# Kernel tuning notes

Measured on AMD Instinct MI355X. Metric: run time of the kernel, lower is better.

The kernel has to match this reference:

```python
import jax, jax.numpy as jnp
import numpy as np

B, N, C = 2, 2048, 1024
H = 16
D = C // H  # 64 head_dim
SCALE = D ** -0.5


def setup_inputs() -> dict:
    key = jax.random.key(0)
    k1, k2, k3 = jax.random.split(key, 3)
    x = jax.random.normal(k1, (B, N, C), dtype=jnp.float32)
    w_qkv = jax.random.normal(k2, (C, 3 * C), dtype=jnp.float32) * (C ** -0.5)
    w_proj = jax.random.normal(k3, (C, C), dtype=jnp.float32) * (C ** -0.5)
    b_proj = jnp.zeros((C,), dtype=jnp.float32)
    return {"x": x, "w_qkv": w_qkv, "w_proj": w_proj, "b_proj": b_proj}


def reference(x, w_qkv, w_proj, b_proj):
    # qkv projection (no bias, qkv_bias=False)
    qkv = x @ w_qkv                                   # [B,N,3C]
    qkv = qkv.reshape(B, N, 3, H, D)
    qkv = jnp.transpose(qkv, (2, 0, 3, 1, 4))         # [3,B,H,N,D]
    q, k, v = qkv[0], qkv[1], qkv[2]
    # scaled dot-product attention (full softmax == chunked loop in original)
    scores = jnp.einsum('bhqd,bhkd->bhqk', q, k) * SCALE
    attn = jax.nn.softmax(scores, axis=-1)
    out = jnp.einsum('bhqk,bhkd->bhqd', attn, v)      # [B,H,N,D]
    out = jnp.transpose(out, (0, 2, 1, 3)).reshape(B, N, C)
    return out @ w_proj + b_proj
```

## Files before the change

kernel.cpp:

```cpp
#include <hip/hip_runtime.h>
#include <stdint.h>

typedef float f32x4 __attribute__((ext_vector_type(4)));
typedef float f32x16 __attribute__((ext_vector_type(16)));
typedef __bf16 bf16x8 __attribute__((ext_vector_type(8)));
typedef unsigned int u32x4 __attribute__((ext_vector_type(4)));
typedef unsigned short u16x4 __attribute__((ext_vector_type(4)));

#define DEV __device__ __forceinline__

#define QSCALE_LOG2E 0.18033688011112042f

DEV unsigned short f2bf(float f) {
    unsigned u = __builtin_bit_cast(unsigned, f);
    u += 0x7fffu + ((u >> 16) & 1u);
    return (unsigned short)(u >> 16);
}

DEV unsigned pack2bf(float a, float b) {
    unsigned short ua = __builtin_bit_cast(unsigned short, (__bf16)a);
    unsigned short ub = __builtin_bit_cast(unsigned short, (__bf16)b);
    return (unsigned)ua | ((unsigned)ub << 16);
}

DEV void pswap(unsigned& a, unsigned& b) {
    asm volatile("v_permlane32_swap_b32 %0, %1" : "+v"(a), "+v"(b));
}

DEV void gload16(const void* g, void* l) {
    __builtin_amdgcn_global_load_lds(
        (const __attribute__((address_space(1))) unsigned int*)(uintptr_t)g,
        (__attribute__((address_space(3))) unsigned int*)(unsigned int)(uintptr_t)l,
        16, 0, 0);
}

__global__ void k_cvt(const float* __restrict__ in, unsigned short* __restrict__ out, int n4) {
    int i = blockIdx.x * 256 + threadIdx.x;
    int st = gridDim.x * 256;
    for (; i < n4; i += st) {
        f32x4 v = *(const f32x4*)(in + (size_t)i * 4);
        u16x4 o;
        o[0] = f2bf(v[0]); o[1] = f2bf(v[1]); o[2] = f2bf(v[2]); o[3] = f2bf(v[3]);
        *(u16x4*)(out + (size_t)i * 4) = o;
    }
}

__global__ void k_transpose(const float* __restrict__ in, unsigned short* __restrict__ out, int Nc) {
    __shared__ unsigned short tl[64][68];
    int n0 = blockIdx.x * 64, k0 = blockIdx.y * 64;
#pragma unroll
    for (int i = 0; i < 16; i++) {
        int idx = i * 256 + threadIdx.x;
        int kr = idx >> 6, nc = idx & 63;
        tl[kr][nc] = f2bf(in[(size_t)(k0 + kr) * Nc + n0 + nc]);
    }
    __syncthreads();
#pragma unroll
    for (int i = 0; i < 8; i++) {
        int idx = i * 256 + threadIdx.x;
        int nr = idx >> 5, kp2 = idx & 31;
        unsigned vv = (unsigned)tl[kp2 * 2][nr] | ((unsigned)tl[kp2 * 2 + 1][nr] << 16);
        *(unsigned*)(out + (size_t)(n0 + nr) * 1024 + k0 + kp2 * 2) = vv;
    }
}

template <int MODE>
__global__ __launch_bounds__(256) void k_gemm(
    const unsigned short* __restrict__ A, const unsigned short* __restrict__ Bt, int K,
    unsigned short* __restrict__ q, unsigned short* __restrict__ kk_,
    unsigned short* __restrict__ vT, const float* __restrict__ bias,
    float* __restrict__ outf) {
    __shared__ unsigned short As[2][128 * 64];
    __shared__ unsigned short Bs[2][128 * 64];
    const int tid = threadIdx.x;
    const int w = tid >> 6, l = tid & 63, g = l >> 4, lr = l & 15;
    const int wr = w >> 1, wc = w & 1;
    const int nwg = gridDim.x * gridDim.y, cpx = nwg >> 3;
    const int lin = blockIdx.y * gridDim.x + blockIdx.x;
    const int swz = (lin & 7) * cpx + (lin >> 3);
    const int m0 = (swz / gridDim.x) * 128, n0 = (swz % gridDim.x) * 128;
    f32x4 acc[4][4] = {};

    auto STAGE = [&](int buf, int k0) {
#pragma unroll
        for (int i = 0; i < 4; i++) {
            int c = i * 256 + tid;
            gload16(A + (size_t)(m0 + (c >> 3)) * K + k0 + (c & 7) * 8, (char*)As[buf] + c * 16);
            gload16(Bt + (size_t)(n0 + (c >> 3)) * K + k0 + (c & 7) * 8, (char*)Bs[buf] + c * 16);
        }
    };

    STAGE(0, 0);
    asm volatile("s_waitcnt vmcnt(0)" ::: "memory");
    __builtin_amdgcn_s_barrier();
    __builtin_amdgcn_sched_barrier(0);

    int cur = 0;
    for (int k0 = 0; k0 < K; k0 += 64) {
        if (k0 + 64 < K) STAGE(cur ^ 1, k0 + 64);
        const unsigned short* Ac = As[cur];
        const unsigned short* Bc = Bs[cur];
#pragma unroll
        for (int kk = 0; kk < 2; kk++) {
            bf16x8 af[4], bfv[4];
#pragma unroll
            for (int mi = 0; mi < 4; mi++)
                af[mi] = *(const bf16x8*)(Ac + (wr * 64 + mi * 16 + lr) * 64 + kk * 32 + g * 8);
#pragma unroll
            for (int ni = 0; ni < 4; ni++)
                bfv[ni] = *(const bf16x8*)(Bc + (wc * 64 + ni * 16 + lr) * 64 + kk * 32 + g * 8);
#pragma unroll
            for (int mi = 0; mi < 4; mi++)
#pragma unroll
                for (int ni = 0; ni < 4; ni++)
                    acc[mi][ni] = __builtin_amdgcn_mfma_f32_16x16x32_bf16(af[mi], bfv[ni], acc[mi][ni], 0, 0, 0);
        }
        asm volatile("s_waitcnt vmcnt(0)" ::: "memory");
        __builtin_amdgcn_s_barrier();
        __builtin_amdgcn_sched_barrier(0);
        cur ^= 1;
    }

#pragma unroll
    for (int mi = 0; mi < 4; mi++) {
#pragma unroll
        for (int ni = 0; ni < 4; ni++) {
            if (MODE == 1) {
                int row0 = m0 + wr * 64 + mi * 16 + g * 4;
                int col = n0 + wc * 64 + ni * 16 + lr;
                int b = row0 >> 11, nn = row0 & 2047;
                int which = col >> 10, cc = col & 1023;
                int h = cc >> 6, d = cc & 63;
                if (which == 2) {
                    u16x4 pv;
#pragma unroll
                    for (int r = 0; r < 4; r++) pv[r] = f2bf(acc[mi][ni][r]);
                    *(u16x4*)&vT[((size_t)(b * 16 + h) * 64 + d) * 2048 + nn] = pv;
                } else {
                    unsigned short* dst = (which == 0) ? q : kk_;
                    const float sc = (which == 0) ? QSCALE_LOG2E : 1.f;
#pragma unroll
                    for (int r = 0; r < 4; r++)
                        dst[((size_t)(b * 16 + h) * 2048 + nn + r) * 64 + d] = f2bf(acc[mi][ni][r] * sc);
                }
            } else {
#pragma unroll
                for (int r = 0; r < 4; r++) {
                    int row = m0 + wr * 64 + mi * 16 + g * 4 + r;
                    int col = n0 + wc * 64 + ni * 16 + lr;
                    outf[(size_t)row * 1024 + col] = acc[mi][ni][r] + bias[col];
                }
            }
        }
    }
}

__global__ __launch_bounds__(512, 2) void k_attn(
    const unsigned short* __restrict__ qb, const unsigned short* __restrict__ kb,
    const unsigned short* __restrict__ vTb, unsigned short* __restrict__ ao) {
    __shared__ __align__(16) char smem[65536];
    const int tid = threadIdx.x;
    const int w = tid >> 6, l = tid & 63, l31 = l & 31, hf = l >> 5;
    const int qg = w & 3, kvh = w >> 2;
    const int bid = blockIdx.x;
    const int xcd = bid & 7, slot = bid >> 3;
    const int bh = xcd * 4 + (slot >> 3), qb_ = slot & 7;
    const int b = bh >> 4, h = bh & 15;
    const unsigned short* qp = qb + (size_t)bh * 131072;
    const unsigned short* kp = kb + (size_t)bh * 131072 + (size_t)kvh * 65536;
    const unsigned short* vTp = vTb + (size_t)bh * 131072 + kvh * 1024;

    const int qrow0 = qb_ * 256 + qg * 64 + l31;
    bf16x8 qf[2][4];
#pragma unroll
    for (int ti = 0; ti < 2; ti++)
#pragma unroll
        for (int dc = 0; dc < 4; dc++)
            qf[ti][dc] = *(const bf16x8*)(qp + (size_t)(qrow0 + ti * 32) * 64 + dc * 16 + hf * 8);
    asm volatile("s_waitcnt vmcnt(0)" ::: "memory");

    f32x16 o_acc[2][2] = {};
    float l_r[2] = {0.f, 0.f};

    const int sr8 = l >> 3;
    const int sco = ((l & 7) ^ sr8) * 8;
    char* sbase = smem + kvh * 32768;
    auto STAGE = [&](char* dst, int kv0) {
#pragma unroll
        for (int i = 0; i < 2; i++) {
            int r = qg + 4 * i;
            gload16(kp + (size_t)(kv0 + r * 8 + sr8) * 64 + sco, dst + r * 1024 + (size_t)l * 16);
            gload16(vTp + (size_t)(r * 8 + sr8) * 2048 + kv0 + sco, dst + 8192 + r * 1024 + (size_t)l * 16);
        }
    };

    STAGE(sbase, 0);
    asm volatile("s_waitcnt vmcnt(0)" ::: "memory");
    __builtin_amdgcn_s_barrier();
    __builtin_amdgcn_sched_barrier(0);

    const int lb = l31 & 7;
    int cur = 0;
    for (int t = 0; t < 16; ++t) {
        if (t < 15) STAGE(sbase + (cur ^ 1) * 16384, (t + 1) * 64);
        const char* p0 = sbase + cur * 16384;

        f32x16 s[2][2] = {};
        __builtin_amdgcn_s_setprio(1);
#pragma unroll
        for (int kt = 0; kt < 2; kt++)
#pragma unroll
            for (int dc = 0; dc < 4; dc++) {
                bf16x8 kf = *(const bf16x8*)(p0 + (kt * 32 + l31) * 128 + (((2 * dc + hf) ^ lb) * 16));
                s[0][kt] = __builtin_amdgcn_mfma_f32_32x32x16_bf16(kf, qf[0][dc], s[0][kt], 0, 0, 0);
                s[1][kt] = __builtin_amdgcn_mfma_f32_32x32x16_bf16(kf, qf[1][dc], s[1][kt], 0, 0, 0);
            }
        __builtin_amdgcn_s_setprio(0);

        bf16x8 pf[2][4];
#pragma unroll
        for (int ti = 0; ti < 2; ti++) {
            float s0 = 0.f, s1 = 0.f, s2 = 0.f, s3 = 0.f;
#pragma unroll
            for (int kt = 0; kt < 2; kt++)
#pragma unroll
                for (int r = 0; r < 16; r += 4) {
                    float e0 = __builtin_amdgcn_exp2f(s[ti][kt][r]);
                    float e1 = __builtin_amdgcn_exp2f(s[ti][kt][r + 1]);
                    float e2 = __builtin_amdgcn_exp2f(s[ti][kt][r + 2]);
                    float e3 = __builtin_amdgcn_exp2f(s[ti][kt][r + 3]);
                    s[ti][kt][r] = e0; s[ti][kt][r + 1] = e1;
                    s[ti][kt][r + 2] = e2; s[ti][kt][r + 3] = e3;
                    s0 += e0; s1 += e1; s2 += e2; s3 += e3;
                }
            float ssum = (s0 + s1) + (s2 + s3);
            ssum += __shfl_xor(ssum, 32);
            l_r[ti] += ssum;
#pragma unroll
            for (int kt = 0; kt < 2; kt++) {
                unsigned wd[8];
#pragma unroll
                for (int i = 0; i < 8; i++)
                    wd[i] = pack2bf(s[ti][kt][2 * i], s[ti][kt][2 * i + 1]);
#pragma unroll
                for (int cl = 0; cl < 2; cl++) {
                    unsigned b0 = wd[4 * cl + 0], b2 = wd[4 * cl + 2];
                    unsigned b1 = wd[4 * cl + 1], b3 = wd[4 * cl + 3];
                    pswap(b0, b2);
                    pswap(b1, b3);
                    u32x4 bw; bw[0] = b0; bw[1] = b1; bw[2] = b2; bw[3] = b3;
                    pf[ti][2 * kt + cl] = __builtin_bit_cast(bf16x8, bw);
                }
            }
        }

        __builtin_amdgcn_s_setprio(1);
#pragma unroll
        for (int c4 = 0; c4 < 4; c4++)
#pragma unroll
            for (int dt = 0; dt < 2; dt++) {
                bf16x8 vf = *(const bf16x8*)(p0 + 8192 + (dt * 32 + l31) * 128 + (((2 * c4 + hf) ^ lb) * 16));
                o_acc[0][dt] = __builtin_amdgcn_mfma_f32_32x32x16_bf16(vf, pf[0][c4], o_acc[0][dt], 0, 0, 0);
                o_acc[1][dt] = __builtin_amdgcn_mfma_f32_32x32x16_bf16(vf, pf[1][c4], o_acc[1][dt], 0, 0, 0);
            }
        __builtin_amdgcn_s_setprio(0);

        if (t < 15) {
            asm volatile("s_waitcnt vmcnt(0)" ::: "memory");
            __builtin_amdgcn_s_barrier();
            __builtin_amdgcn_sched_barrier(0);
        }
        cur ^= 1;
    }

    float* dO = (float*)(smem + qg * 8448);
    float* dL = (float*)(smem + 33792 + qg * 256);
#pragma unroll
    for (int ti = 0; ti < 2; ti++) {
        __syncthreads();
        if (kvh == 1) {
#pragma unroll
            for (int i = 0; i < 16; i++) dO[l * 33 + i] = o_acc[ti][0][i];
#pragma unroll
            for (int i = 0; i < 16; i++) dO[l * 33 + 16 + i] = o_acc[ti][1][i];
            dL[l] = l_r[ti];
        }
        __syncthreads();
        if (kvh == 0) {
            float linv = 1.f / (l_r[ti] + dL[l]);
            unsigned short* aop = ao + ((size_t)b * 2048 + qrow0 + ti * 32) * 1024 + h * 64;
#pragma unroll
            for (int dt = 0; dt < 2; dt++)
#pragma unroll
                for (int rg = 0; rg < 4; rg++) {
                    u16x4 pv;
#pragma unroll
                    for (int k = 0; k < 4; k++) {
                        int r = rg * 4 + k;
                        pv[k] = f2bf((o_acc[ti][dt][r] + dO[l * 33 + dt * 16 + r]) * linv);
                    }
                    *(u16x4*)(aop + 8 * rg + 4 * hf + 32 * dt) = pv;
                }
        }
    }
}

extern "C" void kernel_launch(void* const* d_in, const int* in_sizes, int n_in,
                              void* d_out, int out_size, void* d_ws, size_t ws_size,
                              hipStream_t stream) {
    (void)in_sizes; (void)n_in; (void)out_size; (void)ws_size;
    const float* x      = (const float*)d_in[0];
    const float* w_qkv  = (const float*)d_in[1];
    const float* w_proj = (const float*)d_in[2];
    const float* b_proj = (const float*)d_in[3];
    float* out = (float*)d_out;
    char* ws = (char*)d_ws;

    unsigned short* xb     = (unsigned short*)(ws);
    unsigned short* ao     = (unsigned short*)(ws);
    unsigned short* wqkvT  = (unsigned short*)(ws + 8388608);
    unsigned short* wprojT = (unsigned short*)(ws + 14680064);
    unsigned short* qb     = (unsigned short*)(ws + 16777216);
    unsigned short* kb     = (unsigned short*)(ws + 25165824);
    unsigned short* vTb    = (unsigned short*)(ws + 33554432);

    k_cvt<<<2048, 256, 0, stream>>>(x, xb, 1048576);
    k_transpose<<<dim3(48, 16), 256, 0, stream>>>(w_qkv, wqkvT, 3072);
    k_transpose<<<dim3(16, 16), 256, 0, stream>>>(w_proj, wprojT, 1024);
    k_gemm<1><<<dim3(24, 32), 256, 0, stream>>>(xb, wqkvT, 1024, qb, kb, vTb, nullptr, nullptr);
    k_attn<<<256, 512, 0, stream>>>(qb, kb, vTb, ao);
    k_gemm<3><<<dim3(8, 32), 256, 0, stream>>>(ao, wprojT, 1024, nullptr, nullptr, nullptr, b_proj, out);
}
```

Measured before the change: 120.0 us.

## Load K/V fragments directly from global into registers in attention kernel

```diff
diff --git a/kernel.cpp b/kernel.cpp
--- a/kernel.cpp
+++ b/kernel.cpp
@@ -155,55 +155,49 @@
     }
 }
 
-__global__ __launch_bounds__(512, 2) void k_attn(
+__global__ __launch_bounds__(256, 2) void k_attn(
     const unsigned short* __restrict__ qb, const unsigned short* __restrict__ kb,
     const unsigned short* __restrict__ vTb, unsigned short* __restrict__ ao) {
-    __shared__ __align__(16) char smem[65536];
+    __shared__ float mrg[2][64 * 33 + 64];
     const int tid = threadIdx.x;
     const int w = tid >> 6, l = tid & 63, l31 = l & 31, hf = l >> 5;
-    const int qg = w & 3, kvh = w >> 2;
+    const int qg = w >> 1, kvh = w & 1;
     const int bid = blockIdx.x;
     const int xcd = bid & 7, slot = bid >> 3;
-    const int bh = xcd * 4 + (slot >> 3), qb_ = slot & 7;
+    const int bh = xcd * 4 + (slot >> 4), qb_ = slot & 15;
     const int b = bh >> 4, h = bh & 15;
     const unsigned short* qp = qb + (size_t)bh * 131072;
     const unsigned short* kp = kb + (size_t)bh * 131072 + (size_t)kvh * 65536;
     const unsigned short* vTp = vTb + (size_t)bh * 131072 + kvh * 1024;
 
-    const int qrow0 = qb_ * 256 + qg * 64 + l31;
+    const int qrow0 = qb_ * 128 + qg * 64 + l31;
     bf16x8 qf[2][4];
 #pragma unroll
     for (int ti = 0; ti < 2; ti++)
 #pragma unroll
         for (int dc = 0; dc < 4; dc++)
             qf[ti][dc] = *(const bf16x8*)(qp + (size_t)(qrow0 + ti * 32) * 64 + dc * 16 + hf * 8);
-    asm volatile("s_waitcnt vmcnt(0)" ::: "memory");
 
     f32x16 o_acc[2][2] = {};
     float l_r[2] = {0.f, 0.f};
 
-    const int sr8 = l >> 3;
-    const int sco = ((l & 7) ^ sr8) * 8;
-    char* sbase = smem + kvh * 32768;
-    auto STAGE = [&](char* dst, int kv0) {
-#pragma unroll
-        for (int i = 0; i < 2; i++) {
-            int r = qg + 4 * i;
-            gload16(kp + (size_t)(kv0 + r * 8 + sr8) * 64 + sco, dst + r * 1024 + (size_t)l * 16);
-            gload16(vTp + (size_t)(r * 8 + sr8) * 2048 + kv0 + sco, dst + 8192 + r * 1024 + (size_t)l * 16);
-        }
-    };
-
-    STAGE(sbase, 0);
-    asm volatile("s_waitcnt vmcnt(0)" ::: "memory");
-    __builtin_amdgcn_s_barrier();
-    __builtin_amdgcn_sched_barrier(0);
-
-    const int lb = l31 & 7;
-    int cur = 0;
+    const unsigned short* kbase = kp + (size_t)l31 * 64 + hf * 8;
+    const unsigned short* vbase = vTp + (size_t)l31 * 2048 + hf * 8;
+
+    bf16x8 kf[2][4];
+#pragma unroll
+    for (int kt = 0; kt < 2; kt++)
+#pragma unroll
+        for (int dc = 0; dc < 4; dc++)
+            kf[kt][dc] = *(const bf16x8*)(kbase + kt * 2048 + dc * 16);
+
     for (int t = 0; t < 16; ++t) {
-        if (t < 15) STAGE(sbase + (cur ^ 1) * 16384, (t + 1) * 64);
-        const char* p0 = sbase + cur * 16384;
+        bf16x8 vf[4][2];
+#pragma unroll
+        for (int c4 = 0; c4 < 4; c4++)
+#pragma unroll
+            for (int dt = 0; dt < 2; dt++)
+                vf[c4][dt] = *(const bf16x8*)(vbase + dt * 65536 + t * 64 + c4 * 16);
 
         f32x16 s[2][2] = {};
         __builtin_amdgcn_s_setprio(1);
@@ -211,11 +205,18 @@
         for (int kt = 0; kt < 2; kt++)
 #pragma unroll
             for (int dc = 0; dc < 4; dc++) {
-                bf16x8 kf = *(const bf16x8*)(p0 + (kt * 32 + l31) * 128 + (((2 * dc + hf) ^ lb) * 16));
-                s[0][kt] = __builtin_amdgcn_mfma_f32_32x32x16_bf16(kf, qf[0][dc], s[0][kt], 0, 0, 0);
-                s[1][kt] = __builtin_amdgcn_mfma_f32_32x32x16_bf16(kf, qf[1][dc], s[1][kt], 0, 0, 0);
+                s[0][kt] = __builtin_amdgcn_mfma_f32_32x32x16_bf16(kf[kt][dc], qf[0][dc], s[0][kt], 0, 0, 0);
+                s[1][kt] = __builtin_amdgcn_mfma_f32_32x32x16_bf16(kf[kt][dc], qf[1][dc], s[1][kt], 0, 0, 0);
             }
         __builtin_amdgcn_s_setprio(0);
+
+        if (t < 15) {
+#pragma unroll
+            for (int kt = 0; kt < 2; kt++)
+#pragma unroll
+                for (int dc = 0; dc < 4; dc++)
+                    kf[kt][dc] = *(const bf16x8*)(kbase + (t + 1) * 4096 + kt * 2048 + dc * 16);
+        }
 
         bf16x8 pf[2][4];
 #pragma unroll
@@ -259,22 +260,14 @@
         for (int c4 = 0; c4 < 4; c4++)
 #pragma unroll
             for (int dt = 0; dt < 2; dt++) {
-                bf16x8 vf = *(const bf16x8*)(p0 + 8192 + (dt * 32 + l31) * 128 + (((2 * c4 + hf) ^ lb) * 16));
-                o_acc[0][dt] = __builtin_amdgcn_mfma_f32_32x32x16_bf16(vf, pf[0][c4], o_acc[0][dt], 0, 0, 0);
-                o_acc[1][dt] = __builtin_amdgcn_mfma_f32_32x32x16_bf16(vf, pf[1][c4], o_acc[1][dt], 0, 0, 0);
+                o_acc[0][dt] = __builtin_amdgcn_mfma_f32_32x32x16_bf16(vf[c4][dt], pf[0][c4], o_acc[0][dt], 0, 0, 0);
+                o_acc[1][dt] = __builtin_amdgcn_mfma_f32_32x32x16_bf16(vf[c4][dt], pf[1][c4], o_acc[1][dt], 0, 0, 0);
             }
         __builtin_amdgcn_s_setprio(0);
-
-        if (t < 15) {
-            asm volatile("s_waitcnt vmcnt(0)" ::: "memory");
-            __builtin_amdgcn_s_barrier();
-            __builtin_amdgcn_sched_barrier(0);
-        }
-        cur ^= 1;
-    }
-
-    float* dO = (float*)(smem + qg * 8448);
-    float* dL = (float*)(smem + 33792 + qg * 256);
+    }
+
+    float* dO = mrg[qg];
+    float* dL = mrg[qg] + 64 * 33;
 #pragma unroll
     for (int ti = 0; ti < 2; ti++) {
         __syncthreads();
@@ -328,6 +321,6 @@
     k_transpose<<<dim3(48, 16), 256, 0, stream>>>(w_qkv, wqkvT, 3072);
     k_transpose<<<dim3(16, 16), 256, 0, stream>>>(w_proj, wprojT, 1024);
     k_gemm<1><<<dim3(24, 32), 256, 0, stream>>>(xb, wqkvT, 1024, qb, kb, vTb, nullptr, nullptr);
-    k_attn<<<256, 512, 0, stream>>>(qb, kb, vTb, ao);
+    k_attn<<<512, 256, 0, stream>>>(qb, kb, vTb, ao);
     k_gemm<3><<<dim3(8, 32), 256, 0, stream>>>(ao, wprojT, 1024, nullptr, nullptr, nullptr, b_proj, out);
 }
```

Measured after the change: 155.2 us. 29.3% more time.

## Use 256x256 tiled QKV GEMM with swizzled LDS and interleaved prefetch

Applied to the files above, without the earlier changes.

```diff
diff --git a/kernel.cpp b/kernel.cpp
--- a/kernel.cpp
+++ b/kernel.cpp
@@ -64,12 +64,114 @@
     }
 }
 
-template <int MODE>
-__global__ __launch_bounds__(256) void k_gemm(
+__global__ __launch_bounds__(512, 2) void k_gemm1_256(
     const unsigned short* __restrict__ A, const unsigned short* __restrict__ Bt, int K,
     unsigned short* __restrict__ q, unsigned short* __restrict__ kk_,
-    unsigned short* __restrict__ vT, const float* __restrict__ bias,
-    float* __restrict__ outf) {
+    unsigned short* __restrict__ vT) {
+    __shared__ unsigned short Ab[2][256 * 64];
+    __shared__ unsigned short Bb[2][256 * 64];
+    const int tid = threadIdx.x;
+    const int w = tid >> 6, l = tid & 63, g = l >> 4, lr = l & 15;
+    const int wm = w >> 2, wn = w & 3;
+    const int nwg = gridDim.x * gridDim.y, cpx = nwg >> 3;
+    const int lin = blockIdx.y * gridDim.x + blockIdx.x;
+    const int swz = (lin & 7) * cpx + (lin >> 3);
+    const int m0 = (swz / gridDim.x) * 256, n0 = (swz % gridDim.x) * 256;
+    f32x4 acc[8][4] = {};
+
+    auto SPART = [&](int db, int kt, int i) {
+        int ci = i * 512 + tid;
+        int row = ci >> 3, pos = ci & 7;
+        int gc = (pos ^ (row & 7)) * 8;
+        gload16(A + (size_t)(m0 + row) * K + kt * 64 + gc, (char*)Ab[db] + ci * 16);
+        gload16(Bt + (size_t)(n0 + row) * K + kt * 64 + gc, (char*)Bb[db] + ci * 16);
+    };
+
+#pragma unroll
+    for (int i = 0; i < 4; i++) SPART(0, 0, i);
+    asm volatile("s_waitcnt vmcnt(0)" ::: "memory");
+    __builtin_amdgcn_s_barrier();
+    __builtin_amdgcn_sched_barrier(0);
+
+    const int nt = K >> 6;
+    for (int t = 0; t < nt; ++t) {
+        const int db = t & 1;
+        const char* Ac = (const char*)Ab[db];
+        const char* Bc = (const char*)Bb[db];
+        bf16x8 bfv[4][2];
+#pragma unroll
+        for (int qp = 0; qp < 4; qp++) {
+            if (qp == 0) {
+#pragma unroll
+                for (int ni = 0; ni < 4; ni++)
+#pragma unroll
+                    for (int kk = 0; kk < 2; kk++) {
+                        int row = wn * 64 + ni * 16 + lr;
+                        int c = kk * 4 + g;
+                        bfv[ni][kk] = *(const bf16x8*)(Bc + row * 128 + ((c ^ (row & 7)) * 16));
+                    }
+            }
+            bf16x8 af[2][2];
+#pragma unroll
+            for (int j = 0; j < 2; j++)
+#pragma unroll
+                for (int kk = 0; kk < 2; kk++) {
+                    int row = wm * 128 + (2 * qp + j) * 16 + lr;
+                    int c = kk * 4 + g;
+                    af[j][kk] = *(const bf16x8*)(Ac + row * 128 + ((c ^ (row & 7)) * 16));
+                }
+            if (t < nt - 1 && qp < 2) {
+                SPART(db ^ 1, t + 1, 2 * qp);
+                SPART(db ^ 1, t + 1, 2 * qp + 1);
+            }
+            __builtin_amdgcn_s_barrier();
+            asm volatile("s_waitcnt lgkmcnt(0)" ::: "memory");
+            __builtin_amdgcn_sched_barrier(0);
+            __builtin_amdgcn_s_setprio(1);
+#pragma unroll
+            for (int kk = 0; kk < 2; kk++)
+#pragma unroll
+                for (int j = 0; j < 2; j++)
+#pragma unroll
+                    for (int ni = 0; ni < 4; ni++)
+                        acc[2 * qp + j][ni] = __builtin_amdgcn_mfma_f32_16x16x32_bf16(
+                            af[j][kk], bfv[ni][kk], acc[2 * qp + j][ni], 0, 0, 0);
+            __builtin_amdgcn_s_setprio(0);
+            if (qp == 3 && t < nt - 1)
+                asm volatile("s_waitcnt vmcnt(0)" ::: "memory");
+            __builtin_amdgcn_s_barrier();
+            __builtin_amdgcn_sched_barrier(0);
+        }
+    }
+
+#pragma unroll
+    for (int mi = 0; mi < 8; mi++) {
+#pragma unroll
+        for (int ni = 0; ni < 4; ni++) {
+            int row0 = m0 + wm * 128 + mi * 16 + g * 4;
+            int col = n0 + wn * 64 + ni * 16 + lr;
+            int b = row0 >> 11, nn = row0 & 2047;
+            int which = col >> 10, cc = col & 1023;
+            int h = cc >> 6, d = cc & 63;
+            if (which == 2) {
+                u16x4 pv;
+#pragma unroll
+                for (int r = 0; r < 4; r++) pv[r] = f2bf(acc[mi][ni][r]);
+                *(u16x4*)&vT[((size_t)(b * 16 + h) * 64 + d) * 2048 + nn] = pv;
+            } else {
+                unsigned short* dst = (which == 0) ? q : kk_;
+                const float sc = (which == 0) ? QSCALE_LOG2E : 1.f;
+#pragma unroll
+                for (int r = 0; r < 4; r++)
+                    dst[((size_t)(b * 16 + h) * 2048 + nn + r) * 64 + d] = f2bf(acc[mi][ni][r] * sc);
+            }
+        }
+    }
+}
+
+__global__ __launch_bounds__(256) void k_gemm3(
+    const unsigned short* __restrict__ A, const unsigned short* __restrict__ Bt, int K,
+    const float* __restrict__ bias, float* __restrict__ outf) {
     __shared__ unsigned short As[2][128 * 64];
     __shared__ unsigned short Bs[2][128 * 64];
     const int tid = threadIdx.x;
@@ -122,37 +224,15 @@
     }
 
 #pragma unroll
-    for (int mi = 0; mi < 4; mi++) {
-#pragma unroll
-        for (int ni = 0; ni < 4; ni++) {
-            if (MODE == 1) {
-                int row0 = m0 + wr * 64 + mi * 16 + g * 4;
+    for (int mi = 0; mi < 4; mi++)
+#pragma unroll
+        for (int ni = 0; ni < 4; ni++)
+#pragma unroll
+            for (int r = 0; r < 4; r++) {
+                int row = m0 + wr * 64 + mi * 16 + g * 4 + r;
                 int col = n0 + wc * 64 + ni * 16 + lr;
-                int b = row0 >> 11, nn = row0 & 2047;
-                int which = col >> 10, cc = col & 1023;
-                int h = cc >> 6, d = cc & 63;
-                if (which == 2) {
-                    u16x4 pv;
-#pragma unroll
-                    for (int r = 0; r < 4; r++) pv[r] = f2bf(acc[mi][ni][r]);
-                    *(u16x4*)&vT[((size_t)(b * 16 + h) * 64 + d) * 2048 + nn] = pv;
-                } else {
-                    unsigned short* dst = (which == 0) ? q : kk_;
-                    const float sc = (which == 0) ? QSCALE_LOG2E : 1.f;
-#pragma unroll
-                    for (int r = 0; r < 4; r++)
-                        dst[((size_t)(b * 16 + h) * 2048 + nn + r) * 64 + d] = f2bf(acc[mi][ni][r] * sc);
-                }
-            } else {
-#pragma unroll
-                for (int r = 0; r < 4; r++) {
-                    int row = m0 + wr * 64 + mi * 16 + g * 4 + r;
-                    int col = n0 + wc * 64 + ni * 16 + lr;
-                    outf[(size_t)row * 1024 + col] = acc[mi][ni][r] + bias[col];
-                }
-            }
-        }
-    }
+                outf[(size_t)row * 1024 + col] = acc[mi][ni][r] + bias[col];
+            }
 }
 
 __global__ __launch_bounds__(512, 2) void k_attn(
@@ -327,7 +407,7 @@
     k_cvt<<<2048, 256, 0, stream>>>(x, xb, 1048576);
     k_transpose<<<dim3(48, 16), 256, 0, stream>>>(w_qkv, wqkvT, 3072);
     k_transpose<<<dim3(16, 16), 256, 0, stream>>>(w_proj, wprojT, 1024);
-    k_gemm<1><<<dim3(24, 32), 256, 0, stream>>>(xb, wqkvT, 1024, qb, kb, vTb, nullptr, nullptr);
+    k_gemm1_256<<<dim3(12, 16), 512, 0, stream>>>(xb, wqkvT, 1024, qb, kb, vTb);
     k_attn<<<256, 512, 0, stream>>>(qb, kb, vTb, ao);
-    k_gemm<3><<<dim3(8, 32), 256, 0, stream>>>(ao, wprojT, 1024, nullptr, nullptr, nullptr, b_proj, out);
-}
+    k_gemm3<<<dim3(8, 32), 256, 0, stream>>>(ao, wprojT, 1024, b_proj, out);
+}
```

New measurement: 116.8 us. -2.7%, faster.
